# Kernel optimization log

Measured on AMD Instinct MI355X. Metric: run time of the kernel, lower is better.

The kernel has to match this reference:

```python
import jax, jax.numpy as jnp
import numpy as np

B, NR_BOX, D = 512, 18, 2048
NR_OBJ = NR_BOX - 2
K = 3
NUM_CLASSES = 174
NUM_CAT = 321


def setup_inputs() -> dict:
    key = jax.random.key(0)
    k1, k2, k3, k4, k5, k6 = jax.random.split(key, 6)
    obj_fea = jax.random.normal(k1, (B, NR_BOX, D), dtype=jnp.float32)
    # cooccurrence: nonnegative, sparse-ish, first (pad) column zero as in the torch code
    cooc = jax.random.uniform(k2, (NUM_CLASSES, NUM_CAT), dtype=jnp.float32)
    mask = jax.random.uniform(k3, (NUM_CLASSES, NUM_CAT)) < 0.5
    cooc = jnp.where(mask, cooc, 0.0).at[:, 0].set(0.0)
    obj_indicator = jax.random.randint(k4, (B, NR_BOX), 0, 2).astype(jnp.int32)
    obj_category = jax.random.randint(k5, (B, NR_BOX), 0, NUM_CAT).astype(jnp.int32)
    labels = jax.random.randint(k6, (B,), 0, NUM_CLASSES).astype(jnp.int32)
    return {
        'obj_fea': obj_fea,
        'cooccurrence': cooc,
        'obj_indicator': obj_indicator,
        'obj_category': obj_category,
        'labels': labels,
    }


def reference(obj_fea, cooccurrence, obj_indicator, obj_category, labels):
    Bn, nr_box, d = obj_fea.shape
    nr_obj = nr_box - 2
    ind = obj_indicator[:, 2:]          # (B, nr_obj)
    cats = obj_category[:, 2:]          # (B, nr_obj)
    ori_comp = obj_fea.mean(axis=1)     # (B, d)
    objs = obj_fea[:, 2:]               # (B, nr_obj, d), hands dropped
    label_onehot = jax.nn.one_hot(labels, NUM_CLASSES, dtype=obj_fea.dtype)  # (B, C)

    # W[i, b, j] = cooccurrence[labels[i], cats[b, j]]  (candidate weights per sample i)
    cooc_lab = cooccurrence[labels]                 # (B, NUM_CAT)
    W = cooc_lab[:, cats]                           # (B, B, nr_obj)
    eye = jnp.eye(Bn, dtype=bool)
    W = jnp.where(eye[:, :, None], 0.0, W)          # exclude own video (cand_obj[i] = 0)
    Wf = W.reshape(Bn, Bn * nr_obj)

    # softmax(log w) over nonzero support == w / sum(w); sample via categorical on log-weights
    logits = jnp.where(Wf > 0, jnp.log(jnp.where(Wf > 0, Wf, 1.0)), -jnp.inf)
    has_cand = (Wf > 0).any(axis=1) & (ind != 0).any(axis=1)  # (B,)

    rng = jax.random.key(42)
    r1, r2, r3 = jax.random.split(rng, 3)
    sel = jax.random.categorical(r1, logits, shape=(K, Bn)).T   # (B, K) flat candidate ids
    batch_idx = sel // nr_obj
    box_idx = sel % nr_obj
    sel_fea = objs[batch_idx, box_idx]              # (B, K, d)
    sel_label = label_onehot[batch_idx]             # (B, K, C)

    lam = jax.random.uniform(r2, (Bn, 1, 1), dtype=obj_fea.dtype)  # Beta(1,1)==U(0,1), one per sample
    slots = jax.random.randint(r3, (Bn, K), 0, nr_obj)
    own_fea = jnp.take_along_axis(objs, slots[:, :, None], axis=1)  # (B, K, d)

    mixed_fea = own_fea * lam + sel_fea * (1.0 - lam)
    mixed_label = label_onehot[:, None, :] * lam + sel_label * (1.0 - lam)

    # fallback path: mean of own objects + own one-hot label, repeated K times
    fb_fea = jnp.broadcast_to(objs.mean(axis=1)[:, None, :], mixed_fea.shape)
    fb_label = jnp.broadcast_to(label_onehot[:, None, :], mixed_label.shape)
    m = has_cand[:, None, None]
    mix_fea = jnp.where(m, mixed_fea, fb_fea)
    mix_label = jnp.where(m, mixed_label, fb_label)
    return ori_comp, mix_fea, mix_label
```

## Files before the change

### kernel.cpp

```cpp
#include <hip/hip_runtime.h>
#include <stdint.h>
#include <math.h>

#define NBOX 18
#define BB 512
#define DD 2048
#define NOBJ 16
#define KK 3
#define NCLS 174
#define NCAT 321
#define NSL 16
#define SCAND 512
#define NPART 64

__host__ __device__ __forceinline__ uint32_t rotl32(uint32_t x, int d) {
  return (x << d) | (x >> (32 - d));
}

__host__ __device__ __forceinline__ void threefry2x32(uint32_t k0, uint32_t k1,
                                                      uint32_t x0, uint32_t x1,
                                                      uint32_t& o0, uint32_t& o1) {
  uint32_t ks2 = k0 ^ k1 ^ 0x1BD11BDAu;
  x0 += k0; x1 += k1;
#define TFR(r) x0 += x1; x1 = rotl32(x1, r); x1 ^= x0;
#define R4A TFR(13) TFR(15) TFR(26) TFR(6)
#define R4B TFR(17) TFR(29) TFR(16) TFR(24)
  R4A x0 += k1;  x1 += ks2 + 1u;
  R4B x0 += ks2; x1 += k0 + 2u;
  R4A x0 += k0;  x1 += k1 + 3u;
  R4B x0 += k1;  x1 += ks2 + 4u;
  R4A x0 += ks2; x1 += k0 + 5u;
#undef R4A
#undef R4B
#undef TFR
  o0 = x0; o1 = x1;
}

__device__ __forceinline__ float bits_to_unit(uint32_t bits) {
  float f = __uint_as_float((bits >> 9) | 0x3f800000u);
  return f - 1.0f;
}

__device__ __forceinline__ void gload_lds16(const void* g, void* l) {
  __builtin_amdgcn_global_load_lds(
      (const __attribute__((address_space(1))) unsigned int*)g,
      (__attribute__((address_space(3))) unsigned int*)l, 16, 0, 0);
}

__global__ __launch_bounds__(256) void sample_stream_kernel(
    const float* __restrict__ obj_fea, const float* __restrict__ cooc,
    const int* __restrict__ obj_cat, const int* __restrict__ labels,
    uint32_t r1h, uint32_t r1l,
    unsigned long long* __restrict__ part, int* __restrict__ cnts,
    float* __restrict__ ori, float4* __restrict__ m16ws) {
  const int gb = blockIdx.x;
  const int b = gb >> 4;
  const int o = gb & 15;
  const int tid = threadIdx.x;
  const int lane = tid & 63;
  const int wid = tid >> 6;

  __shared__ float4 slds[NBOX * 32];
  __shared__ unsigned short jl[SCAND];
  __shared__ float wl[SCAND];

  const int col0 = o << 5;
  const float4* fea4 = (const float4*)obj_fea;
  {
    const float4* gbase = fea4 + (size_t)b * NBOX * 512 + col0;
    for (int i = wid; i < 9; i += 4) {
      const float4* g = gbase + (size_t)(2 * i + (lane >> 5)) * 512 + (lane & 31);
      gload_lds16((const void*)g, (void*)((char*)slds + i * 1024));
    }
  }
  __builtin_amdgcn_sched_barrier(0);

  const int lab = labels[b];
  const float* crow = cooc + (size_t)lab * NCAT;
  const int seg = wid << 7;
  const int jbase = (o << 9) + seg;
  int cnt = 0;
#pragma unroll 1
  for (int c = 0; c < 2; ++c) {
    int j = jbase + (c << 6) + lane;
    int jb = j >> 4;
    float w = 0.0f;
    if (jb != b) w = crow[obj_cat[jb * NBOX + 2 + (j & 15)]];
    unsigned long long m = __ballot(w > 0.0f);
    if (w > 0.0f) {
      int rank = __popcll(m & ((1ull << lane) - 1ull));
      jl[seg + cnt + rank] = (unsigned short)j;
      wl[seg + cnt + rank] = w;
    }
    cnt += __popcll(m);
  }

  const uint32_t cbase0 = ((uint32_t)b) << 13;
  const uint32_t kstep = 1u << 22;
  float bw0 = 0.f, bt0 = 1.f, bw1 = 0.f, bt1 = 1.f, bw2 = 0.f, bt2 = 1.f;
  int bj0 = 0, bj1 = 0, bj2 = 0;
#pragma unroll 1
  for (int p = lane; p < cnt; p += 64) {
    uint32_t j = jl[seg + p];
    float w = wl[seg + p];
    uint32_t cc = cbase0 + j;
    uint32_t x0, x1, y0, y1, z0, z1;
    threefry2x32(r1h, r1l, 0u, cc, x0, x1);
    threefry2x32(r1h, r1l, 0u, cc + kstep, y0, y1);
    threefry2x32(r1h, r1l, 0u, cc + 2u * kstep, z0, z1);
    float t0 = -__log2f(fmaxf(bits_to_unit(x0 ^ x1), 1.1920929e-07f));
    float t1 = -__log2f(fmaxf(bits_to_unit(y0 ^ y1), 1.1920929e-07f));
    float t2 = -__log2f(fmaxf(bits_to_unit(z0 ^ z1), 1.1920929e-07f));
    if (w * bt0 > bw0 * t0) { bw0 = w; bt0 = t0; bj0 = (int)j; }
    if (w * bt1 > bw1 * t1) { bw1 = w; bt1 = t1; bj1 = (int)j; }
    if (w * bt2 > bw2 * t2) { bw2 = w; bt2 = t2; bj2 = (int)j; }
  }
#pragma unroll
  for (int mm = 1; mm < 64; mm <<= 1) {
    float ow, ot; int oj;
    ow = __shfl_xor(bw0, mm, 64); ot = __shfl_xor(bt0, mm, 64); oj = __shfl_xor(bj0, mm, 64);
    { float lv = ow * bt0, rv = bw0 * ot;
      if (lv > rv || (lv == rv && oj < bj0)) { bw0 = ow; bt0 = ot; bj0 = oj; } }
    ow = __shfl_xor(bw1, mm, 64); ot = __shfl_xor(bt1, mm, 64); oj = __shfl_xor(bj1, mm, 64);
    { float lv = ow * bt1, rv = bw1 * ot;
      if (lv > rv || (lv == rv && oj < bj1)) { bw1 = ow; bt1 = ot; bj1 = oj; } }
    ow = __shfl_xor(bw2, mm, 64); ot = __shfl_xor(bt2, mm, 64); oj = __shfl_xor(bj2, mm, 64);
    { float lv = ow * bt2, rv = bw2 * ot;
      if (lv > rv || (lv == rv && oj < bj2)) { bw2 = ow; bt2 = ot; bj2 = oj; } }
  }
  if (lane == 0) {
    const int pw = (o << 2) + wid;
    const size_t pb = (size_t)b * KK * NPART;
    part[pb + 0 * NPART + pw] =
        ((unsigned long long)__float_as_uint(bw0 / bt0) << 32) | (uint32_t)(8192 - bj0);
    part[pb + 1 * NPART + pw] =
        ((unsigned long long)__float_as_uint(bw1 / bt1) << 32) | (uint32_t)(8192 - bj1);
    part[pb + 2 * NPART + pw] =
        ((unsigned long long)__float_as_uint(bw2 / bt2) << 32) | (uint32_t)(8192 - bj2);
    cnts[b * NPART + pw] = cnt;
  }

  __syncthreads();
  if (wid == 0) {
    const int col = lane & 31;
    const int rh = lane >> 5;
    float4 acc = make_float4(0.f, 0.f, 0.f, 0.f);
    float4 v0 = acc, v1 = acc;
#pragma unroll
    for (int r = 0; r < 9; ++r) {
      float4 t = slds[(rh * 9 + r) * 32 + col];
      if (r == 0) v0 = t;
      if (r == 1) v1 = t;
      acc.x += t.x; acc.y += t.y; acc.z += t.z; acc.w += t.w;
    }
    float4 oth;
    oth.x = __shfl_xor(acc.x, 32, 64); oth.y = __shfl_xor(acc.y, 32, 64);
    oth.z = __shfl_xor(acc.z, 32, 64); oth.w = __shfl_xor(acc.w, 32, 64);
    if (rh == 0) {
      float4 S = make_float4(acc.x + oth.x, acc.y + oth.y, acc.z + oth.z, acc.w + oth.w);
      const float i18 = 1.0f / 18.0f, i16 = 1.0f / 16.0f;
      const size_t oidx = (size_t)b * 512 + col0 + col;
      ((float4*)ori)[oidx] = make_float4(S.x * i18, S.y * i18, S.z * i18, S.w * i18);
      m16ws[oidx] = make_float4((S.x - v0.x - v1.x) * i16, (S.y - v0.y - v1.y) * i16,
                                (S.z - v0.z - v1.z) * i16, (S.w - v0.w - v1.w) * i16);
    }
  }
}

__global__ __launch_bounds__(256) void mix_kernel(
    const float* __restrict__ obj_fea, const int* __restrict__ obj_ind,
    const int* __restrict__ labels,
    const unsigned long long* __restrict__ part, const int* __restrict__ cnts,
    const float4* __restrict__ m16ws,
    uint32_t r2h, uint32_t r2l, uint32_t r3bh, uint32_t r3bl,
    float* __restrict__ mixf, float* __restrict__ mixl) {
  const int bx = blockIdx.x;
  const int b = bx >> 1;
  const int h = bx & 1;
  const int tid = threadIdx.x;
  const int off = (h << 8) + tid;

  __shared__ int s_sel[KK];
  __shared__ int s_slots[KK];
  __shared__ float s_lam;
  __shared__ int s_cnt;
  __shared__ int s_any;

  if (tid < 64) {
    unsigned long long p0 = part[((size_t)b * KK + 0) * NPART + tid];
    unsigned long long p1 = part[((size_t)b * KK + 1) * NPART + tid];
    unsigned long long p2 = part[((size_t)b * KK + 2) * NPART + tid];
    int ct = cnts[b * NPART + tid];
#pragma unroll
    for (int mm = 1; mm < 64; mm <<= 1) {
      unsigned long long q;
      q = __shfl_xor(p0, mm, 64); if (q > p0) p0 = q;
      q = __shfl_xor(p1, mm, 64); if (q > p1) p1 = q;
      q = __shfl_xor(p2, mm, 64); if (q > p2) p2 = q;
      ct |= __shfl_xor(ct, mm, 64);
    }
    if (tid == 0) {
      s_sel[0] = 8192 - (int)(p0 & 0xFFFFFFFFull);
      s_sel[1] = 8192 - (int)(p1 & 0xFFFFFFFFull);
      s_sel[2] = 8192 - (int)(p2 & 0xFFFFFFFFull);
      s_cnt = ct;
    }
  } else if (tid < 67) {
    const int k = tid - 64;
    uint32_t s0, s1;
    threefry2x32(r3bh, r3bl, 0u, (uint32_t)(b * KK + k), s0, s1);
    s_slots[k] = (int)((s0 ^ s1) & 15u);
  } else if (tid == 67) {
    uint32_t c0, c1;
    threefry2x32(r2h, r2l, 0u, (uint32_t)b, c0, c1);
    s_lam = bits_to_unit(c0 ^ c1);
  } else if (tid == 68) {
    int any = 0;
#pragma unroll
    for (int oo = 0; oo < NOBJ; ++oo) any |= (obj_ind[b * NBOX + 2 + oo] != 0);
    s_any = any;
  }
  __syncthreads();

  const int hc = (s_cnt != 0) && s_any;
  const float l = s_lam, l1 = 1.0f - l;
  const float4* fea4 = (const float4*)obj_fea;
  float4* mixf4 = (float4*)mixf;
  if (hc) {
#pragma unroll 1
    for (int k = 0; k < KK; ++k) {
      int s = s_sel[k];
      int bi = s >> 4, bo = s & 15, sl = s_slots[k];
      float4 a = fea4[((size_t)b * NBOX + 2 + sl) * 512 + off];
      float4 e = fea4[((size_t)bi * NBOX + 2 + bo) * 512 + off];
      float4 ov;
      ov.x = a.x * l + e.x * l1; ov.y = a.y * l + e.y * l1;
      ov.z = a.z * l + e.z * l1; ov.w = a.w * l + e.w * l1;
      mixf4[((size_t)b * KK + k) * 512 + off] = ov;
    }
  } else {
    float4 m16 = m16ws[(size_t)b * 512 + off];
#pragma unroll
    for (int k = 0; k < KK; ++k) mixf4[((size_t)b * KK + k) * 512 + off] = m16;
  }

  if (h == 0 && tid < NCLS) {
    int lb = labels[b];
#pragma unroll 1
    for (int k = 0; k < KK; ++k) {
      float val;
      if (hc) {
        int ls = labels[s_sel[k] >> 4];
        val = (tid == lb ? l : 0.0f) + (tid == ls ? l1 : 0.0f);
      } else {
        val = (tid == lb) ? 1.0f : 0.0f;
      }
      mixl[(size_t)(b * KK + k) * NCLS + tid] = val;
    }
  }
}

extern "C" void kernel_launch(void* const* d_in, const int* in_sizes, int n_in,
                              void* d_out, int out_size, void* d_ws, size_t ws_size,
                              hipStream_t stream) {
  (void)in_sizes; (void)n_in; (void)out_size; (void)ws_size;
  const float* obj_fea = (const float*)d_in[0];
  const float* cooc    = (const float*)d_in[1];
  const int* obj_ind   = (const int*)d_in[2];
  const int* obj_cat   = (const int*)d_in[3];
  const int* labels    = (const int*)d_in[4];

  float* out  = (float*)d_out;
  float* ori  = out;
  float* mixf = out + (size_t)BB * DD;
  float* mixl = mixf + (size_t)BB * KK * DD;

  char* ws = (char*)d_ws;
  unsigned long long* part = (unsigned long long*)ws;
  int* cnts = (int*)(ws + (size_t)BB * KK * NPART * 8);
  float4* m16ws = (float4*)(ws + 1024 * 1024);

  uint32_t r1h, r1l, r2h, r2l, r3h, r3l;
  threefry2x32(0u, 42u, 0u, 0u, r1h, r1l);
  threefry2x32(0u, 42u, 0u, 1u, r2h, r2l);
  threefry2x32(0u, 42u, 0u, 2u, r3h, r3l);
  uint32_t r3bh, r3bl;
  threefry2x32(r3h, r3l, 0u, 1u, r3bh, r3bl);

  hipLaunchKernelGGL(sample_stream_kernel, dim3(BB * NSL), dim3(256), 0, stream,
                     obj_fea, cooc, obj_cat, labels, r1h, r1l,
                     part, cnts, ori, m16ws);
  hipLaunchKernelGGL(mix_kernel, dim3(BB * 2), dim3(256), 0, stream,
                     obj_fea, obj_ind, labels, part, cnts, m16ws,
                     r2h, r2l, r3bh, r3bl, mixf, mixl);
}
```

Baseline: 52.41 us.

## Coarsen sampling kernel to four blocks per sample with wider column tiles

Each sample is now handled by 4 blocks instead of 16. Every block covers 2048 candidates and 128 float4 columns of the feature mean, and all four waves take part in the column reduction instead of only wave 0. The mix kernel reduces over 16 partials instead of 64. The aim is to cut block-launch overhead and per-block fixed costs such as the label lookup, the ballot compaction and the RNG setup. In exchange each block has fewer blocks running alongside it, a longer serial candidate loop and larger LDS use.

```diff
diff --git a/kernel.cpp b/kernel.cpp
--- a/kernel.cpp
+++ b/kernel.cpp
@@ -9,9 +9,9 @@
 #define KK 3
 #define NCLS 174
 #define NCAT 321
-#define NSL 16
-#define SCAND 512
-#define NPART 64
+#define NQ 4
+#define QCAND 2048
+#define NPART 16
 
 __host__ __device__ __forceinline__ uint32_t rotl32(uint32_t x, int d) {
   return (x << d) | (x >> (32 - d));
@@ -54,34 +54,35 @@
     unsigned long long* __restrict__ part, int* __restrict__ cnts,
     float* __restrict__ ori, float4* __restrict__ m16ws) {
   const int gb = blockIdx.x;
-  const int b = gb >> 4;
-  const int o = gb & 15;
+  const int b = gb >> 2;
+  const int q = gb & 3;
   const int tid = threadIdx.x;
   const int lane = tid & 63;
   const int wid = tid >> 6;
 
-  __shared__ float4 slds[NBOX * 32];
-  __shared__ unsigned short jl[SCAND];
-  __shared__ float wl[SCAND];
-
-  const int col0 = o << 5;
+  __shared__ float4 slds[NBOX * 128];
+  __shared__ unsigned short jl[QCAND];
+  __shared__ float wl[QCAND];
+
+  const int col0 = q << 7;
   const float4* fea4 = (const float4*)obj_fea;
-  {
-    const float4* gbase = fea4 + (size_t)b * NBOX * 512 + col0;
-    for (int i = wid; i < 9; i += 4) {
-      const float4* g = gbase + (size_t)(2 * i + (lane >> 5)) * 512 + (lane & 31);
-      gload_lds16((const void*)g, (void*)((char*)slds + i * 1024));
-    }
+  const float4* gbase = fea4 + (size_t)b * NBOX * 512 + col0;
+#pragma unroll
+  for (int i = 0; i < 9; ++i) {
+    const int L = wid * 9 + i;
+    const int r = L >> 1, hh = L & 1;
+    const float4* g = gbase + (size_t)r * 512 + hh * 64 + lane;
+    gload_lds16((const void*)g, (void*)((char*)slds + (size_t)L * 1024));
   }
   __builtin_amdgcn_sched_barrier(0);
 
   const int lab = labels[b];
   const float* crow = cooc + (size_t)lab * NCAT;
-  const int seg = wid << 7;
-  const int jbase = (o << 9) + seg;
+  const int seg = wid << 9;
+  const int jbase = (q << 11) + seg;
   int cnt = 0;
 #pragma unroll 1
-  for (int c = 0; c < 2; ++c) {
+  for (int c = 0; c < 8; ++c) {
     int j = jbase + (c << 6) + lane;
     int jb = j >> 4;
     float w = 0.0f;
@@ -129,7 +130,7 @@
       if (lv > rv || (lv == rv && oj < bj2)) { bw2 = ow; bt2 = ot; bj2 = oj; } }
   }
   if (lane == 0) {
-    const int pw = (o << 2) + wid;
+    const int pw = (q << 2) + wid;
     const size_t pb = (size_t)b * KK * NPART;
     part[pb + 0 * NPART + pw] =
         ((unsigned long long)__float_as_uint(bw0 / bt0) << 32) | (uint32_t)(8192 - bj0);
@@ -141,29 +142,26 @@
   }
 
   __syncthreads();
-  if (wid == 0) {
-    const int col = lane & 31;
-    const int rh = lane >> 5;
-    float4 acc = make_float4(0.f, 0.f, 0.f, 0.f);
-    float4 v0 = acc, v1 = acc;
-#pragma unroll
-    for (int r = 0; r < 9; ++r) {
-      float4 t = slds[(rh * 9 + r) * 32 + col];
-      if (r == 0) v0 = t;
-      if (r == 1) v1 = t;
-      acc.x += t.x; acc.y += t.y; acc.z += t.z; acc.w += t.w;
-    }
-    float4 oth;
-    oth.x = __shfl_xor(acc.x, 32, 64); oth.y = __shfl_xor(acc.y, 32, 64);
-    oth.z = __shfl_xor(acc.z, 32, 64); oth.w = __shfl_xor(acc.w, 32, 64);
-    if (rh == 0) {
-      float4 S = make_float4(acc.x + oth.x, acc.y + oth.y, acc.z + oth.z, acc.w + oth.w);
-      const float i18 = 1.0f / 18.0f, i16 = 1.0f / 16.0f;
-      const size_t oidx = (size_t)b * 512 + col0 + col;
-      ((float4*)ori)[oidx] = make_float4(S.x * i18, S.y * i18, S.z * i18, S.w * i18);
-      m16ws[oidx] = make_float4((S.x - v0.x - v1.x) * i16, (S.y - v0.y - v1.y) * i16,
-                                (S.z - v0.z - v1.z) * i16, (S.w - v0.w - v1.w) * i16);
-    }
+  const int rh = tid & 1;
+  const int col = tid >> 1;
+  float4 acc = make_float4(0.f, 0.f, 0.f, 0.f);
+#pragma unroll
+  for (int r = 0; r < 9; ++r) {
+    float4 t = slds[(rh * 9 + r) * 128 + col];
+    acc.x += t.x; acc.y += t.y; acc.z += t.z; acc.w += t.w;
+  }
+  float4 oth;
+  oth.x = __shfl_xor(acc.x, 1, 64); oth.y = __shfl_xor(acc.y, 1, 64);
+  oth.z = __shfl_xor(acc.z, 1, 64); oth.w = __shfl_xor(acc.w, 1, 64);
+  if (rh == 0) {
+    float4 S = make_float4(acc.x + oth.x, acc.y + oth.y, acc.z + oth.z, acc.w + oth.w);
+    float4 v0 = slds[col];
+    float4 v1 = slds[128 + col];
+    const float i18 = 1.0f / 18.0f, i16 = 1.0f / 16.0f;
+    const size_t oidx = (size_t)b * 512 + col0 + col;
+    ((float4*)ori)[oidx] = make_float4(S.x * i18, S.y * i18, S.z * i18, S.w * i18);
+    m16ws[oidx] = make_float4((S.x - v0.x - v1.x) * i16, (S.y - v0.y - v1.y) * i16,
+                              (S.z - v0.z - v1.z) * i16, (S.w - v0.w - v1.w) * i16);
   }
 }
 
@@ -186,17 +184,17 @@
   __shared__ int s_cnt;
   __shared__ int s_any;
 
-  if (tid < 64) {
+  if (tid < NPART) {
     unsigned long long p0 = part[((size_t)b * KK + 0) * NPART + tid];
     unsigned long long p1 = part[((size_t)b * KK + 1) * NPART + tid];
     unsigned long long p2 = part[((size_t)b * KK + 2) * NPART + tid];
     int ct = cnts[b * NPART + tid];
 #pragma unroll
-    for (int mm = 1; mm < 64; mm <<= 1) {
-      unsigned long long q;
-      q = __shfl_xor(p0, mm, 64); if (q > p0) p0 = q;
-      q = __shfl_xor(p1, mm, 64); if (q > p1) p1 = q;
-      q = __shfl_xor(p2, mm, 64); if (q > p2) p2 = q;
+    for (int mm = 1; mm < NPART; mm <<= 1) {
+      unsigned long long qq;
+      qq = __shfl_xor(p0, mm, 64); if (qq > p0) p0 = qq;
+      qq = __shfl_xor(p1, mm, 64); if (qq > p1) p1 = qq;
+      qq = __shfl_xor(p2, mm, 64); if (qq > p2) p2 = qq;
       ct |= __shfl_xor(ct, mm, 64);
     }
     if (tid == 0) {
@@ -205,16 +203,16 @@
       s_sel[2] = 8192 - (int)(p2 & 0xFFFFFFFFull);
       s_cnt = ct;
     }
-  } else if (tid < 67) {
-    const int k = tid - 64;
+  } else if (tid < NPART + KK) {
+    const int k = tid - NPART;
     uint32_t s0, s1;
     threefry2x32(r3bh, r3bl, 0u, (uint32_t)(b * KK + k), s0, s1);
     s_slots[k] = (int)((s0 ^ s1) & 15u);
-  } else if (tid == 67) {
+  } else if (tid == NPART + KK) {
     uint32_t c0, c1;
     threefry2x32(r2h, r2l, 0u, (uint32_t)b, c0, c1);
     s_lam = bits_to_unit(c0 ^ c1);
-  } else if (tid == 68) {
+  } else if (tid == NPART + KK + 1) {
     int any = 0;
 #pragma unroll
     for (int oo = 0; oo < NOBJ; ++oo) any |= (obj_ind[b * NBOX + 2 + oo] != 0);
@@ -287,7 +285,7 @@
   uint32_t r3bh, r3bl;
   threefry2x32(r3h, r3l, 0u, 1u, r3bh, r3bl);
 
-  hipLaunchKernelGGL(sample_stream_kernel, dim3(BB * NSL), dim3(256), 0, stream,
+  hipLaunchKernelGGL(sample_stream_kernel, dim3(BB * NQ), dim3(256), 0, stream,
                      obj_fea, cooc, obj_cat, labels, r1h, r1l,
                      part, cnts, ori, m16ws);
   hipLaunchKernelGGL(mix_kernel, dim3(BB * 2), dim3(256), 0, stream,
```

Measured after the change: 48.49 us. -7.5%, faster.
